# Kernel optimization log

Hardware: AMD Instinct MI355X
Metric: run time of the kernel (lower is better)

## Reference

```python
import jax, jax.numpy as jnp
import numpy as np

B, N, F, Tf, Tm, Df, Dm = 8, 128, 128, 64, 256, 32, 128
E, H, TE = 64, 128, 64  # node_emb_dim, hidden_dim, time_emb_dim


def setup_inputs() -> dict:
    key = jax.random.key(0)
    ks = jax.random.split(key, 16)
    s = 0.05
    return {
        'noisy_adj': jax.random.normal(ks[0], (B, N, N), jnp.float32),
        'node_feats': jax.random.normal(ks[1], (B, N, F), jnp.float32),
        'feat_fnirs': jax.random.normal(ks[2], (B, N, Tf, Df), jnp.float32),
        'feat_music': jax.random.normal(ks[3], (B, 1, Tm, Dm), jnp.float32),
        'g_pre': jax.random.normal(ks[4], (B, N, N), jnp.float32),
        'node_W': jax.random.normal(ks[5], (F, E), jnp.float32) * s,
        'node_b': jnp.zeros((E,), jnp.float32),
        'fnirs_W': jax.random.normal(ks[6], (Df, H), jnp.float32) * s,
        'fnirs_b': jnp.zeros((H,), jnp.float32),
        'music_W': jax.random.normal(ks[7], (Dm, H), jnp.float32) * s,
        'music_b': jnp.zeros((H,), jnp.float32),
        'mlp_W1': jax.random.normal(ks[8], (2 * E + 2 + H + TE, H), jnp.float32) * s,
        'mlp_b1': jnp.zeros((H,), jnp.float32),
        'mlp_W2': jax.random.normal(ks[9], (H, 1), jnp.float32) * s,
        'mlp_b2': jnp.zeros((1,), jnp.float32),
        't': jax.random.randint(ks[10], (B,), 0, Tf),
    }


def _time_embedding(t_idx):
    # sinusoidal timestep embedding -> [B, TE]
    half = TE // 2
    inv_freq = jnp.exp(-jnp.arange(half, dtype=jnp.float32) * (jnp.log(10000.0) / (half - 1)))
    freqs = t_idx.astype(jnp.float32)[:, None] * inv_freq  # [B, half]
    return jnp.concatenate([jnp.sin(freqs), jnp.cos(freqs)], axis=-1)


def _conditional(feat_fnirs, feat_music, fnirs_W, fnirs_b, music_W, music_b):
    # cross-attention: fNIRS timesteps attend over music timesteps
    q = feat_fnirs @ fnirs_W + fnirs_b          # [B,N,Tf,H]
    kv = feat_music @ music_W + music_b         # [B,1,Tm,H]
    scale = 1.0 / jnp.sqrt(jnp.float32(H))
    scores = jnp.einsum('bnfh,bomh->bnfm', q, kv) * scale  # [B,N,Tf,Tm]
    attn = jax.nn.softmax(scores, axis=-1)
    ctx = jnp.einsum('bnfm,bomh->bnfh', attn, kv)
    fused = q + ctx                              # [B,N,Tf,H]
    attn_weights = attn.mean(axis=1)             # mean across channels -> [B,Tf,Tm]
    ent = -(attn * jnp.log(attn + 1e-8)).sum(-1)
    attention_loss = ent.mean()
    return fused, attn_weights, attention_loss


def reference(noisy_adj, node_feats, feat_fnirs, feat_music, g_pre,
              node_W, node_b, fnirs_W, fnirs_b, music_W, music_b,
              mlp_W1, mlp_b1, mlp_W2, mlp_b2, t):
    h = node_feats @ node_W + node_b             # [B,N,E]

    fused, attn_weights, attention_loss = _conditional(
        feat_fnirs, feat_music, fnirs_W, fnirs_b, music_W, music_b)

    t_idx = jnp.clip(t, 0, fused.shape[2] - 1)
    # gather conditional state at diffusion step t -> [B,N,H]
    idx = jnp.broadcast_to(t_idx[:, None, None, None], (B, N, 1, H))
    cond_t = jnp.take_along_axis(fused, idx, axis=2)[:, :, 0, :]

    time_emb = _time_embedding(t_idx)            # [B,TE]

    # Fused edge MLP layer-1: split W1 along the concat axis instead of
    # materializing the [B,N,N,in_dim] concat tensor (same math).
    W1_hi = mlp_W1[:E]
    W1_hj = mlp_W1[E:2 * E]
    w_adj = mlp_W1[2 * E]          # [H]
    w_gpre = mlp_W1[2 * E + 1]     # [H]
    W1_cond = mlp_W1[2 * E + 2:2 * E + 2 + H]
    W1_time = mlp_W1[2 * E + 2 + H:]

    pre = ((h @ W1_hi)[:, :, None, :]            # h_i varies over row i
           + (h @ W1_hj)[:, None, :, :]          # h_j varies over col j
           + noisy_adj[..., None] * w_adj
           + g_pre[..., None] * w_gpre
           + (cond_t @ W1_cond)[:, None, :, :]   # cond broadcast over row i
           + (time_emb @ W1_time)[:, None, None, :]
           + mlp_b1)                             # [B,N,N,H]
    hid = jax.nn.relu(pre)
    noise_pred = (hid @ mlp_W2)[..., 0] + mlp_b2[0]  # [B,N,N]
    return noise_pred, attn_weights, attention_loss
```

## Files before the change

kernel.cpp:

```cpp
#include <hip/hip_runtime.h>
#include <hip/hip_bf16.h>

#define Bn  8
#define Nn  128
#define Fn  128
#define Tfn 64
#define Tmn 256
#define Dfn 32
#define Dmn 128
#define En  64
#define Hn  128
#define TEn 64

#define OUT_AW_OFF   (Bn*Nn*Nn)
#define OUT_LOSS_OFF (Bn*Nn*Nn + Bn*Tfn*Tmn)

#define WS_G     0
#define WS_BIAS  32768
#define WS_KVT   34816
#define WS_FWT   165888
#define WS_NWT   167936
#define WS_HIT   172032
#define WS_HJT   176128
#define WS_CONDT 180224
#define WS_TVEC  188416
#define WS_PI    189440
#define WS_PJ    320512
#define WS_LOSS  451584

#define SCALE 0.08838834764831845f

typedef __attribute__((ext_vector_type(8))) short short8;
typedef __attribute__((ext_vector_type(4))) float f32x4;

__device__ __forceinline__ unsigned short f2bf(float x) {
  __hip_bfloat16 h = __float2bfloat16(x);
  return __builtin_bit_cast(unsigned short, h);
}
__device__ __forceinline__ unsigned int pk2(float a, float b) {
  return (unsigned int)f2bf(a) | ((unsigned int)f2bf(b) << 16);
}

__global__ __launch_bounds__(128) void k_wprep(
    const float* __restrict__ W1, const float* __restrict__ b1,
    const float* __restrict__ node_W, const float* __restrict__ fnirs_W,
    const int* __restrict__ t,
    unsigned short* __restrict__ fwt, unsigned short* __restrict__ nwt,
    unsigned short* __restrict__ hit, unsigned short* __restrict__ hjt,
    unsigned short* __restrict__ condt, float* __restrict__ tvec,
    float* __restrict__ loss_acc)
{
  int blk = blockIdx.x, tid = threadIdx.x;
  if (blk < 8) {
    int b = blk;
    __shared__ float te_l[TEn];
    if (tid < TEn/2) {
      int tcl = min(max(t[b], 0), Tfn - 1);
      float fr = (float)tcl * __expf(-(float)tid * (logf(10000.f) / (TEn/2 - 1)));
      te_l[tid] = __sinf(fr);
      te_l[tid + TEn/2] = __cosf(fr);
    }
    __syncthreads();
    float a = b1[tid];
    #pragma unroll 8
    for (int u = 0; u < TEn; u++) a = fmaf(te_l[u], W1[(2*En + 2 + Hn + u)*Hn + tid], a);
    tvec[b*Hn + tid] = a;
    if (b == 0 && tid == 0) loss_acc[0] = 0.f;
  } else if (blk < 16) {
    int q = blk - 8;
    #pragma unroll 4
    for (int i = 0; i < 16; i++) {
      int k = q*16 + i;
      condt[k*Hn + tid] = f2bf(W1[(2*En + 2 + tid)*Hn + k]);
    }
  } else if (blk < 20) {
    int q = blk - 16;
    int e = tid & 63, kh = tid >> 6;
    #pragma unroll 4
    for (int i = 0; i < 16; i++) {
      int k = q*32 + kh*16 + i;
      hit[k*En + e] = f2bf(W1[e*Hn + k]);
    }
  } else if (blk < 24) {
    int q = blk - 20;
    int e = tid & 63, kh = tid >> 6;
    #pragma unroll 4
    for (int i = 0; i < 16; i++) {
      int k = q*32 + kh*16 + i;
      hjt[k*En + e] = f2bf(W1[(En + e)*Hn + k]);
    }
  } else if (blk < 32) {
    int q = blk - 24;
    int fl = tid & 15, eh = tid >> 4;
    #pragma unroll 4
    for (int i = 0; i < 8; i++) {
      int e = eh*8 + i;
      nwt[e*Fn + q*16 + fl] = f2bf(node_W[(q*16 + fl)*En + e]);
    }
  } else if (blk < 34) {
    int q = blk - 32;
    int d = tid & 31, hh = tid >> 5;
    #pragma unroll 4
    for (int i = 0; i < 16; i++) {
      int h = q*64 + hh*16 + i;
      fwt[h*Dfn + d] = f2bf(fnirs_W[d*Hn + h]);
    }
  }
}

__global__ __launch_bounds__(128) void k_kv(
    const float* __restrict__ feat_music, const float* __restrict__ music_W,
    const float* __restrict__ music_b, const float* __restrict__ fnirs_W,
    const float* __restrict__ fnirs_b, unsigned short* __restrict__ kvT,
    unsigned short* __restrict__ G_bf, float* __restrict__ bias)
{
  int b = blockIdx.x >> 8;
  int m = blockIdx.x & 255;
  int tid = threadIdx.x;
  __shared__ float fm_s[Dmn];
  __shared__ float kv_s[Hn];
  __shared__ float red[2];
  fm_s[tid] = feat_music[((size_t)b*Tmn + m)*Dmn + tid];
  __syncthreads();
  float a = music_b[tid];
  #pragma unroll 8
  for (int d = 0; d < Dmn; d++) a = fmaf(fm_s[d], music_W[d*Hn + tid], a);
  kv_s[tid] = a;
  kvT[((size_t)b*Hn + tid)*Tmn + m] = f2bf(a);
  float bp = fnirs_b[tid] * a;
  bp += __shfl_xor(bp, 32); bp += __shfl_xor(bp, 16); bp += __shfl_xor(bp, 8);
  bp += __shfl_xor(bp, 4);  bp += __shfl_xor(bp, 2);  bp += __shfl_xor(bp, 1);
  if ((tid & 63) == 0) red[tid >> 6] = bp;
  __syncthreads();
  int d = tid >> 2, qd = tid & 3;
  float g = 0.f;
  #pragma unroll 8
  for (int hh = 0; hh < 32; hh++) {
    int h = hh*4 + qd;
    g = fmaf(fnirs_W[d*Hn + h], kv_s[h], g);
  }
  g += __shfl_xor(g, 1); g += __shfl_xor(g, 2);
  if (qd == 0) G_bf[((size_t)b*Tmn + m)*Dfn + d] = f2bf(g * SCALE);
  if (tid == 0) bias[b*Tmn + m] = (red[0] + red[1]) * SCALE;
}

__global__ __launch_bounds__(256, 2) void k_attn(
    const float* __restrict__ feat_fnirs, const unsigned short* __restrict__ G_bf,
    const float* __restrict__ bias, float* __restrict__ aw_out,
    float* __restrict__ loss_acc)
{
  __shared__ unsigned short feat_l[Nn][40];
  __shared__ unsigned short G_l[Tmn][40];
  __shared__ float bias_l[Tmn];
  __shared__ float aw_l[4][Tmn];
  __shared__ float ent_l[4];

  int tid = threadIdx.x;
  int b = blockIdx.x >> 6, f = blockIdx.x & 63;

  {
    const uint4* gg = (const uint4*)(G_bf + (size_t)b*Tmn*Dfn);
    #pragma unroll
    for (int v0 = 0; v0 < 4; v0++) {
      int v = tid + v0*256;
      uint4 x = gg[v];
      int m = v >> 2, qt = v & 3;
      *((uint4*)&G_l[m][qt*8]) = x;
    }
    bias_l[tid] = bias[b*Tmn + tid];
    int n = tid >> 1, hf = tid & 1;
    const float* src = feat_fnirs + (((size_t)b*Nn + n)*Tfn + f)*Dfn + hf*16;
    float4 x0 = ((const float4*)src)[0];
    float4 x1 = ((const float4*)src)[1];
    float4 x2 = ((const float4*)src)[2];
    float4 x3 = ((const float4*)src)[3];
    uint4 pa, pb;
    pa.x = pk2(x0.x, x0.y); pa.y = pk2(x0.z, x0.w);
    pa.z = pk2(x1.x, x1.y); pa.w = pk2(x1.z, x1.w);
    pb.x = pk2(x2.x, x2.y); pb.y = pk2(x2.z, x2.w);
    pb.z = pk2(x3.x, x3.y); pb.w = pk2(x3.z, x3.w);
    uint4* dst = (uint4*)&feat_l[n][hf*16];
    dst[0] = pa; dst[1] = pb;
  }
  __syncthreads();

  int lane = tid & 63, wv = tid >> 6;
  int col = lane & 15, kq = lane >> 4;
  int n0 = wv * 32;

  short8 a0 = *(const short8*)&feat_l[n0 + col][kq*8];
  short8 a1 = *(const short8*)&feat_l[n0 + 16 + col][kq*8];

  float S0[4] = {0,0,0,0}, S1[4] = {0,0,0,0};
  float T0[4] = {0,0,0,0}, T1[4] = {0,0,0,0};
  float p0[16][4], p1[16][4];

  #pragma unroll
  for (int mt = 0; mt < 16; mt++) {
    short8 bfr = *(const short8*)&G_l[mt*16 + col][kq*8];
    float bv = bias_l[mt*16 + col];
    f32x4 c0 = __builtin_amdgcn_mfma_f32_16x16x32_bf16(a0, bfr, (f32x4){0.f,0.f,0.f,0.f}, 0, 0, 0);
    f32x4 c1 = __builtin_amdgcn_mfma_f32_16x16x32_bf16(a1, bfr, (f32x4){0.f,0.f,0.f,0.f}, 0, 0, 0);
    #pragma unroll
    for (int r = 0; r < 4; r++) {
      float sc = c0[r] + bv;
      float p = __expf(sc);
      S0[r] += p; T0[r] = fmaf(p, sc, T0[r]); p0[mt][r] = p;
      sc = c1[r] + bv;
      p = __expf(sc);
      S1[r] += p; T1[r] = fmaf(p, sc, T1[r]); p1[mt][r] = p;
    }
  }

  #pragma unroll
  for (int r = 0; r < 4; r++) {
    #pragma unroll
    for (int off = 1; off < 16; off <<= 1) {
      S0[r] += __shfl_xor(S0[r], off);
      S1[r] += __shfl_xor(S1[r], off);
      T0[r] += __shfl_xor(T0[r], off);
      T1[r] += __shfl_xor(T1[r], off);
    }
  }
  float i0v[4], i1v[4];
  #pragma unroll
  for (int r = 0; r < 4; r++) { i0v[r] = 1.f / S0[r]; i1v[r] = 1.f / S1[r]; }

  float ent = 0.f;
  if (col == 0) {
    #pragma unroll
    for (int r = 0; r < 4; r++) {
      ent += (__logf(S0[r]) - T0[r] * i0v[r]);
      ent += (__logf(S1[r]) - T1[r] * i1v[r]);
    }
  }
  ent += __shfl_xor(ent, 32); ent += __shfl_xor(ent, 16);
  ent += __shfl_xor(ent, 8);  ent += __shfl_xor(ent, 4);
  ent += __shfl_xor(ent, 2);  ent += __shfl_xor(ent, 1);
  if (lane == 0) ent_l[wv] = ent;

  #pragma unroll
  for (int mt = 0; mt < 16; mt++) {
    float a = 0.f;
    #pragma unroll
    for (int r = 0; r < 4; r++) {
      a = fmaf(p0[mt][r], i0v[r], a);
      a = fmaf(p1[mt][r], i1v[r], a);
    }
    a += __shfl_xor(a, 16);
    a += __shfl_xor(a, 32);
    if (lane < 16) aw_l[wv][mt*16 + lane] = a;
  }
  __syncthreads();

  float s = (aw_l[0][tid] + aw_l[1][tid]) + (aw_l[2][tid] + aw_l[3][tid]);
  aw_out[((size_t)b*Tfn + f)*Tmn + tid] = s * (1.f/(float)Nn);
  if (tid == 0)
    atomicAdd(loss_acc, (ent_l[0] + ent_l[1]) + (ent_l[2] + ent_l[3]));
}

__global__ __launch_bounds__(256) void k_cond(
    const float* __restrict__ feat_fnirs, const float* __restrict__ node_feats,
    const float* __restrict__ node_b, const int* __restrict__ t,
    const unsigned short* __restrict__ G_bf, const float* __restrict__ bias,
    const unsigned short* __restrict__ kvT, const unsigned short* __restrict__ fwt,
    const unsigned short* __restrict__ nwt, const unsigned short* __restrict__ hit,
    const unsigned short* __restrict__ hjt, const unsigned short* __restrict__ condt,
    const float* __restrict__ tvec, float* __restrict__ Pi, float* __restrict__ Pj)
{
  __shared__ unsigned short featT_l[16][40];
  __shared__ unsigned short A_l[16][264];
  __shared__ unsigned short nf_l[16][136];
  __shared__ unsigned short h_l[16][72];
  __shared__ unsigned short cond_l[16][136];
  __shared__ float sS[4][16];
  __shared__ float tvec_l[Hn];

  int tid = threadIdx.x;
  int b = blockIdx.x >> 3;
  int i0 = (blockIdx.x & 7) << 4;
  int tcl = min(max(t[b], 0), Tfn - 1);

  if (tid < 128) {
    int i = tid >> 3, c = (tid & 7) * 4;
    const float* src = feat_fnirs + (((size_t)b*Nn + i0 + i)*Tfn + tcl)*Dfn + c;
    float4 x = *(const float4*)src;
    *(unsigned int*)&featT_l[i][c]     = pk2(x.x, x.y);
    *(unsigned int*)&featT_l[i][c + 2] = pk2(x.z, x.w);
    tvec_l[tid] = tvec[b*Hn + tid];
  }
  {
    int i = tid >> 4, c = (tid & 15) * 8;
    const float* src = node_feats + ((size_t)b*Nn + i0 + i)*Fn + c;
    float4 x0 = ((const float4*)src)[0];
    float4 x1 = ((const float4*)src)[1];
    *(unsigned int*)&nf_l[i][c]     = pk2(x0.x, x0.y);
    *(unsigned int*)&nf_l[i][c + 2] = pk2(x0.z, x0.w);
    *(unsigned int*)&nf_l[i][c + 4] = pk2(x1.x, x1.y);
    *(unsigned int*)&nf_l[i][c + 6] = pk2(x1.z, x1.w);
  }
  __syncthreads();

  int lane = tid & 63, wv = tid >> 6;
  int col = lane & 15, kq = lane >> 4;

  short8 a_feat = *(const short8*)&featT_l[col][kq*8];

  float p[4][4];
  float Sp[4] = {0,0,0,0};
  #pragma unroll
  for (int mtl = 0; mtl < 4; mtl++) {
    int mt = wv*4 + mtl;
    short8 bg = *(const short8*)(G_bf + ((size_t)b*Tmn + mt*16 + col)*Dfn + kq*8);
    f32x4 c = __builtin_amdgcn_mfma_f32_16x16x32_bf16(a_feat, bg, (f32x4){0.f,0.f,0.f,0.f}, 0, 0, 0);
    float bv = bias[b*Tmn + mt*16 + col];
    #pragma unroll
    for (int r = 0; r < 4; r++) {
      float pp = __expf(c[r] + bv);
      p[mtl][r] = pp;
      Sp[r] += pp;
    }
  }
  #pragma unroll
  for (int r = 0; r < 4; r++) {
    float v = Sp[r];
    v += __shfl_xor(v, 1); v += __shfl_xor(v, 2);
    v += __shfl_xor(v, 4); v += __shfl_xor(v, 8);
    Sp[r] = v;
  }
  if (col == 0) {
    #pragma unroll
    for (int r = 0; r < 4; r++) sS[wv][kq*4 + r] = Sp[r];
  }
  __syncthreads();
  float invS[4];
  #pragma unroll
  for (int r = 0; r < 4; r++)
    invS[r] = 1.f / (sS[0][kq*4+r] + sS[1][kq*4+r] + sS[2][kq*4+r] + sS[3][kq*4+r]);
  #pragma unroll
  for (int mtl = 0; mtl < 4; mtl++) {
    #pragma unroll
    for (int r = 0; r < 4; r++)
      A_l[kq*4 + r][(wv*4 + mtl)*16 + col] = f2bf(p[mtl][r] * invS[r]);
  }
  __syncthreads();

  f32x4 accC0 = {0.f,0.f,0.f,0.f}, accC1 = {0.f,0.f,0.f,0.f};
  {
    int ct0 = wv*2, ct1 = wv*2 + 1;
    short8 bq0 = *(const short8*)(fwt + (size_t)(ct0*16 + col)*Dfn + kq*8);
    short8 bq1 = *(const short8*)(fwt + (size_t)(ct1*16 + col)*Dfn + kq*8);
    accC0 = __builtin_amdgcn_mfma_f32_16x16x32_bf16(a_feat, bq0, accC0, 0, 0, 0);
    accC1 = __builtin_amdgcn_mfma_f32_16x16x32_bf16(a_feat, bq1, accC1, 0, 0, 0);
    #pragma unroll
    for (int ks = 0; ks < 8; ks++) {
      short8 aA = *(const short8*)&A_l[col][ks*32 + kq*8];
      short8 bk0 = *(const short8*)(kvT + ((size_t)b*Hn + ct0*16 + col)*Tmn + ks*32 + kq*8);
      short8 bk1 = *(const short8*)(kvT + ((size_t)b*Hn + ct1*16 + col)*Tmn + ks*32 + kq*8);
      accC0 = __builtin_amdgcn_mfma_f32_16x16x32_bf16(aA, bk0, accC0, 0, 0, 0);
      accC1 = __builtin_amdgcn_mfma_f32_16x16x32_bf16(aA, bk1, accC1, 0, 0, 0);
    }
  }
  f32x4 accH = {0.f,0.f,0.f,0.f};
  #pragma unroll
  for (int ks = 0; ks < 4; ks++) {
    short8 aN = *(const short8*)&nf_l[col][ks*32 + kq*8];
    short8 bn = *(const short8*)(nwt + (size_t)(wv*16 + col)*Fn + ks*32 + kq*8);
    accH = __builtin_amdgcn_mfma_f32_16x16x32_bf16(aN, bn, accH, 0, 0, 0);
  }
  float nb = node_b[wv*16 + col];
  #pragma unroll
  for (int r = 0; r < 4; r++) {
    cond_l[kq*4 + r][(wv*2    )*16 + col] = f2bf(accC0[r]);
    cond_l[kq*4 + r][(wv*2 + 1)*16 + col] = f2bf(accC1[r]);
    h_l[kq*4 + r][wv*16 + col] = f2bf(accH[r] + nb);
  }
  __syncthreads();

  short8 aH[2];
  aH[0] = *(const short8*)&h_l[col][kq*8];
  aH[1] = *(const short8*)&h_l[col][32 + kq*8];
  #pragma unroll
  for (int ctl = 0; ctl < 2; ctl++) {
    int ct = wv*2 + ctl;
    f32x4 accPi = {0.f,0.f,0.f,0.f}, accPj = {0.f,0.f,0.f,0.f};
    #pragma unroll
    for (int ks = 0; ks < 2; ks++) {
      short8 bi_ = *(const short8*)(hit + (size_t)(ct*16 + col)*En + ks*32 + kq*8);
      short8 bj_ = *(const short8*)(hjt + (size_t)(ct*16 + col)*En + ks*32 + kq*8);
      accPi = __builtin_amdgcn_mfma_f32_16x16x32_bf16(aH[ks], bi_, accPi, 0, 0, 0);
      accPj = __builtin_amdgcn_mfma_f32_16x16x32_bf16(aH[ks], bj_, accPj, 0, 0, 0);
    }
    #pragma unroll
    for (int ks = 0; ks < 4; ks++) {
      short8 aC = *(const short8*)&cond_l[col][ks*32 + kq*8];
      short8 bc = *(const short8*)(condt + (size_t)(ct*16 + col)*Hn + ks*32 + kq*8);
      accPj = __builtin_amdgcn_mfma_f32_16x16x32_bf16(aC, bc, accPj, 0, 0, 0);
    }
    float tv = tvec_l[ct*16 + col];
    #pragma unroll
    for (int r = 0; r < 4; r++) {
      size_t row = (size_t)b*Nn + i0 + kq*4 + r;
      Pi[row*Hn + ct*16 + col] = accPi[r];
      Pj[row*Hn + ct*16 + col] = accPj[r] + tv;
    }
  }
}

__global__ __launch_bounds__(256) void k_edge(
    const float* __restrict__ adj, const float* __restrict__ gpre,
    const float* __restrict__ W1, const float* __restrict__ W2,
    const float* __restrict__ b2p, const float* __restrict__ Pi,
    const float* __restrict__ Pj, float* __restrict__ out,
    const float* __restrict__ loss_acc)
{
  int b  = blockIdx.x >> 6;
  int ib = (blockIdx.x >> 1) & 31;
  int jh = blockIdx.x & 1;
  int i0 = ib * 4;
  int tid = threadIdx.x;

  __shared__ float4 Pj_s4[64*32];
  __shared__ float4 Pi_s4[4*32];
  __shared__ float4 w2_s[32], wa_s[32], wg_s[32];

  {
    const float4* Pjg = (const float4*)(Pj + ((size_t)b*Nn + jh*64)*Hn);
    #pragma unroll
    for (int v0 = 0; v0 < 8; v0++) {
      int idx = tid + v0*256;
      int j = idx >> 5, c = idx & 31;
      Pj_s4[j*32 + (c ^ (j & 7))] = Pjg[j*32 + c];
    }
    if (tid < 128) {
      int r = tid >> 5, c = tid & 31;
      Pi_s4[r*32 + c] = ((const float4*)(Pi + ((size_t)b*Nn + i0 + r)*Hn))[c];
    } else if (tid < 160) {
      int c = tid - 128;
      w2_s[c] = ((const float4*)W2)[c];
      wa_s[c] = ((const float4*)(W1 + (2*En)*Hn))[c];
      wg_s[c] = ((const float4*)(W1 + (2*En + 1)*Hn))[c];
    }
  }
  __syncthreads();

  int r = tid >> 6, lane = tid & 63;
  int i = i0 + r, j = jh*64 + lane;
  float b2v = b2p[0];
  float adjv = adj [((size_t)b*Nn + i)*Nn + j];
  float gpv  = gpre[((size_t)b*Nn + i)*Nn + j];
  float a0 = 0.f, a1 = 0.f, a2 = 0.f, a3 = 0.f;
  #pragma unroll
  for (int c = 0; c < 32; c++) {
    float4 pj = Pj_s4[lane*32 + (c ^ (lane & 7))];
    float4 pi = Pi_s4[r*32 + c];
    float4 wa = wa_s[c], wg = wg_s[c], w2 = w2_s[c];
    float e0 = pi.x + pj.x + adjv*wa.x + gpv*wg.x;
    float e1 = pi.y + pj.y + adjv*wa.y + gpv*wg.y;
    float e2 = pi.z + pj.z + adjv*wa.z + gpv*wg.z;
    float e3 = pi.w + pj.w + adjv*wa.w + gpv*wg.w;
    a0 = fmaf(fmaxf(e0, 0.f), w2.x, a0);
    a1 = fmaf(fmaxf(e1, 0.f), w2.y, a1);
    a2 = fmaf(fmaxf(e2, 0.f), w2.z, a2);
    a3 = fmaf(fmaxf(e3, 0.f), w2.w, a3);
  }
  out[((size_t)b*Nn + i)*Nn + j] = (a0 + a1) + (a2 + a3) + b2v;

  if (blockIdx.x == 0 && tid == 0)
    out[OUT_LOSS_OFF] = loss_acc[0] * (1.f / (float)(Bn*Nn*Tfn));
}

extern "C" void kernel_launch(void* const* d_in, const int* in_sizes, int n_in,
                              void* d_out, int out_size, void* d_ws, size_t ws_size,
                              hipStream_t stream) {
  (void)in_sizes; (void)n_in; (void)out_size; (void)ws_size;
  const float* noisy_adj  = (const float*)d_in[0];
  const float* node_feats = (const float*)d_in[1];
  const float* feat_fnirs = (const float*)d_in[2];
  const float* feat_music = (const float*)d_in[3];
  const float* g_pre      = (const float*)d_in[4];
  const float* node_W     = (const float*)d_in[5];
  const float* node_b     = (const float*)d_in[6];
  const float* fnirs_W    = (const float*)d_in[7];
  const float* fnirs_b    = (const float*)d_in[8];
  const float* music_W    = (const float*)d_in[9];
  const float* music_b    = (const float*)d_in[10];
  const float* mlp_W1     = (const float*)d_in[11];
  const float* mlp_b1     = (const float*)d_in[12];
  const float* mlp_W2     = (const float*)d_in[13];
  const float* mlp_b2     = (const float*)d_in[14];
  const int*   t          = (const int*)d_in[15];

  float* out = (float*)d_out;
  float* ws = (float*)d_ws;
  unsigned short* g_ws    = (unsigned short*)(ws + WS_G);
  float*          bias_ws = ws + WS_BIAS;
  unsigned short* kvt_ws  = (unsigned short*)(ws + WS_KVT);
  unsigned short* fwt_ws  = (unsigned short*)(ws + WS_FWT);
  unsigned short* nwt_ws  = (unsigned short*)(ws + WS_NWT);
  unsigned short* hit_ws  = (unsigned short*)(ws + WS_HIT);
  unsigned short* hjt_ws  = (unsigned short*)(ws + WS_HJT);
  unsigned short* cndt_ws = (unsigned short*)(ws + WS_CONDT);
  float*          tvec_ws = ws + WS_TVEC;
  float*          Pi_ws   = ws + WS_PI;
  float*          Pj_ws   = ws + WS_PJ;
  float*          loss_ws = ws + WS_LOSS;

  k_wprep<<<34,         128, 0, stream>>>(mlp_W1, mlp_b1, node_W, fnirs_W, t,
                                          fwt_ws, nwt_ws, hit_ws, hjt_ws, cndt_ws,
                                          tvec_ws, loss_ws);
  k_kv   <<<Bn*Tmn,     128, 0, stream>>>(feat_music, music_W, music_b, fnirs_W,
                                          fnirs_b, kvt_ws, g_ws, bias_ws);
  k_attn <<<Bn*Tfn,     256, 0, stream>>>(feat_fnirs, g_ws, bias_ws,
                                          out + OUT_AW_OFF, loss_ws);
  k_cond <<<Bn*(Nn/16), 256, 0, stream>>>(feat_fnirs, node_feats, node_b, t,
                                          g_ws, bias_ws, kvt_ws, fwt_ws, nwt_ws,
                                          hit_ws, hjt_ws, cndt_ws, tvec_ws,
                                          Pi_ws, Pj_ws);
  k_edge <<<512,        256, 0, stream>>>(noisy_adj, g_pre, mlp_W1, mlp_W2, mlp_b2,
                                          Pi_ws, Pj_ws, out, loss_ws);
}
```

Measured before the change: 137.1 us.

## Merge independent kernels into combined launches and widen edge LDS swizzle

The five launches become three. The weight-prep blocks and the music KV projection blocks now share one grid, and the attention-weights blocks share a grid with the conditional-state blocks, with shared memory overlaid through a union. The aim is to cut launch overhead and let independent work run concurrently on the GPU. The edge kernel's Pj shared-memory XOR swizzle now uses all 5 lane bits instead of 3 to reduce LDS bank conflicts. Merging attention with conditional state puts both branches under one register and occupancy budget, and the union forces the larger shared-memory footprint on every block.

```diff
diff --git a/kernel.cpp b/kernel.cpp
--- a/kernel.cpp
+++ b/kernel.cpp
@@ -41,19 +41,56 @@
   return (unsigned int)f2bf(a) | ((unsigned int)f2bf(b) << 16);
 }
 
-__global__ __launch_bounds__(128) void k_wprep(
+__global__ __launch_bounds__(128) void k_prep(
+    const float* __restrict__ feat_music, const float* __restrict__ music_W,
+    const float* __restrict__ music_b, const float* __restrict__ fnirs_W,
+    const float* __restrict__ fnirs_b,
     const float* __restrict__ W1, const float* __restrict__ b1,
-    const float* __restrict__ node_W, const float* __restrict__ fnirs_W,
-    const int* __restrict__ t,
+    const float* __restrict__ node_W, const int* __restrict__ t,
+    unsigned short* __restrict__ kvT, unsigned short* __restrict__ G_bf,
+    float* __restrict__ bias,
     unsigned short* __restrict__ fwt, unsigned short* __restrict__ nwt,
     unsigned short* __restrict__ hit, unsigned short* __restrict__ hjt,
     unsigned short* __restrict__ condt, float* __restrict__ tvec,
     float* __restrict__ loss_acc)
 {
-  int blk = blockIdx.x, tid = threadIdx.x;
+  __shared__ float fm_s[Dmn];
+  __shared__ float kv_s[Hn];
+  __shared__ float red[2];
+  __shared__ float te_l[TEn];
+  int tid = threadIdx.x;
+
+  if (blockIdx.x < 2048) {
+    int b = blockIdx.x >> 8;
+    int m = blockIdx.x & 255;
+    fm_s[tid] = feat_music[((size_t)b*Tmn + m)*Dmn + tid];
+    __syncthreads();
+    float a = music_b[tid];
+    #pragma unroll 8
+    for (int d = 0; d < Dmn; d++) a = fmaf(fm_s[d], music_W[d*Hn + tid], a);
+    kv_s[tid] = a;
+    kvT[((size_t)b*Hn + tid)*Tmn + m] = f2bf(a);
+    float bp = fnirs_b[tid] * a;
+    bp += __shfl_xor(bp, 32); bp += __shfl_xor(bp, 16); bp += __shfl_xor(bp, 8);
+    bp += __shfl_xor(bp, 4);  bp += __shfl_xor(bp, 2);  bp += __shfl_xor(bp, 1);
+    if ((tid & 63) == 0) red[tid >> 6] = bp;
+    __syncthreads();
+    int d = tid >> 2, qd = tid & 3;
+    float g = 0.f;
+    #pragma unroll 8
+    for (int hh = 0; hh < 32; hh++) {
+      int h = hh*4 + qd;
+      g = fmaf(fnirs_W[d*Hn + h], kv_s[h], g);
+    }
+    g += __shfl_xor(g, 1); g += __shfl_xor(g, 2);
+    if (qd == 0) G_bf[((size_t)b*Tmn + m)*Dfn + d] = f2bf(g * SCALE);
+    if (tid == 0) bias[b*Tmn + m] = (red[0] + red[1]) * SCALE;
+    return;
+  }
+
+  int blk = blockIdx.x - 2048;
   if (blk < 8) {
     int b = blk;
-    __shared__ float te_l[TEn];
     if (tid < TEn/2) {
       int tcl = min(max(t[b], 0), Tfn - 1);
       float fr = (float)tcl * __expf(-(float)tid * (logf(10000.f) / (TEn/2 - 1)));
@@ -108,203 +145,171 @@
   }
 }
 
-__global__ __launch_bounds__(128) void k_kv(
-    const float* __restrict__ feat_music, const float* __restrict__ music_W,
-    const float* __restrict__ music_b, const float* __restrict__ fnirs_W,
-    const float* __restrict__ fnirs_b, unsigned short* __restrict__ kvT,
-    unsigned short* __restrict__ G_bf, float* __restrict__ bias)
-{
-  int b = blockIdx.x >> 8;
-  int m = blockIdx.x & 255;
-  int tid = threadIdx.x;
-  __shared__ float fm_s[Dmn];
-  __shared__ float kv_s[Hn];
-  __shared__ float red[2];
-  fm_s[tid] = feat_music[((size_t)b*Tmn + m)*Dmn + tid];
-  __syncthreads();
-  float a = music_b[tid];
-  #pragma unroll 8
-  for (int d = 0; d < Dmn; d++) a = fmaf(fm_s[d], music_W[d*Hn + tid], a);
-  kv_s[tid] = a;
-  kvT[((size_t)b*Hn + tid)*Tmn + m] = f2bf(a);
-  float bp = fnirs_b[tid] * a;
-  bp += __shfl_xor(bp, 32); bp += __shfl_xor(bp, 16); bp += __shfl_xor(bp, 8);
-  bp += __shfl_xor(bp, 4);  bp += __shfl_xor(bp, 2);  bp += __shfl_xor(bp, 1);
-  if ((tid & 63) == 0) red[tid >> 6] = bp;
-  __syncthreads();
-  int d = tid >> 2, qd = tid & 3;
-  float g = 0.f;
-  #pragma unroll 8
-  for (int hh = 0; hh < 32; hh++) {
-    int h = hh*4 + qd;
-    g = fmaf(fnirs_W[d*Hn + h], kv_s[h], g);
-  }
-  g += __shfl_xor(g, 1); g += __shfl_xor(g, 2);
-  if (qd == 0) G_bf[((size_t)b*Tmn + m)*Dfn + d] = f2bf(g * SCALE);
-  if (tid == 0) bias[b*Tmn + m] = (red[0] + red[1]) * SCALE;
-}
-
-__global__ __launch_bounds__(256, 2) void k_attn(
-    const float* __restrict__ feat_fnirs, const unsigned short* __restrict__ G_bf,
-    const float* __restrict__ bias, float* __restrict__ aw_out,
-    float* __restrict__ loss_acc)
-{
-  __shared__ unsigned short feat_l[Nn][40];
-  __shared__ unsigned short G_l[Tmn][40];
-  __shared__ float bias_l[Tmn];
-  __shared__ float aw_l[4][Tmn];
-  __shared__ float ent_l[4];
-
-  int tid = threadIdx.x;
-  int b = blockIdx.x >> 6, f = blockIdx.x & 63;
-
-  {
-    const uint4* gg = (const uint4*)(G_bf + (size_t)b*Tmn*Dfn);
-    #pragma unroll
-    for (int v0 = 0; v0 < 4; v0++) {
-      int v = tid + v0*256;
-      uint4 x = gg[v];
-      int m = v >> 2, qt = v & 3;
-      *((uint4*)&G_l[m][qt*8]) = x;
-    }
-    bias_l[tid] = bias[b*Tmn + tid];
-    int n = tid >> 1, hf = tid & 1;
-    const float* src = feat_fnirs + (((size_t)b*Nn + n)*Tfn + f)*Dfn + hf*16;
-    float4 x0 = ((const float4*)src)[0];
-    float4 x1 = ((const float4*)src)[1];
-    float4 x2 = ((const float4*)src)[2];
-    float4 x3 = ((const float4*)src)[3];
-    uint4 pa, pb;
-    pa.x = pk2(x0.x, x0.y); pa.y = pk2(x0.z, x0.w);
-    pa.z = pk2(x1.x, x1.y); pa.w = pk2(x1.z, x1.w);
-    pb.x = pk2(x2.x, x2.y); pb.y = pk2(x2.z, x2.w);
-    pb.z = pk2(x3.x, x3.y); pb.w = pk2(x3.z, x3.w);
-    uint4* dst = (uint4*)&feat_l[n][hf*16];
-    dst[0] = pa; dst[1] = pb;
-  }
-  __syncthreads();
-
-  int lane = tid & 63, wv = tid >> 6;
-  int col = lane & 15, kq = lane >> 4;
-  int n0 = wv * 32;
-
-  short8 a0 = *(const short8*)&feat_l[n0 + col][kq*8];
-  short8 a1 = *(const short8*)&feat_l[n0 + 16 + col][kq*8];
-
-  float S0[4] = {0,0,0,0}, S1[4] = {0,0,0,0};
-  float T0[4] = {0,0,0,0}, T1[4] = {0,0,0,0};
-  float p0[16][4], p1[16][4];
-
-  #pragma unroll
-  for (int mt = 0; mt < 16; mt++) {
-    short8 bfr = *(const short8*)&G_l[mt*16 + col][kq*8];
-    float bv = bias_l[mt*16 + col];
-    f32x4 c0 = __builtin_amdgcn_mfma_f32_16x16x32_bf16(a0, bfr, (f32x4){0.f,0.f,0.f,0.f}, 0, 0, 0);
-    f32x4 c1 = __builtin_amdgcn_mfma_f32_16x16x32_bf16(a1, bfr, (f32x4){0.f,0.f,0.f,0.f}, 0, 0, 0);
-    #pragma unroll
-    for (int r = 0; r < 4; r++) {
-      float sc = c0[r] + bv;
-      float p = __expf(sc);
-      S0[r] += p; T0[r] = fmaf(p, sc, T0[r]); p0[mt][r] = p;
-      sc = c1[r] + bv;
-      p = __expf(sc);
-      S1[r] += p; T1[r] = fmaf(p, sc, T1[r]); p1[mt][r] = p;
-    }
-  }
-
-  #pragma unroll
-  for (int r = 0; r < 4; r++) {
-    #pragma unroll
-    for (int off = 1; off < 16; off <<= 1) {
-      S0[r] += __shfl_xor(S0[r], off);
-      S1[r] += __shfl_xor(S1[r], off);
-      T0[r] += __shfl_xor(T0[r], off);
-      T1[r] += __shfl_xor(T1[r], off);
-    }
-  }
-  float i0v[4], i1v[4];
-  #pragma unroll
-  for (int r = 0; r < 4; r++) { i0v[r] = 1.f / S0[r]; i1v[r] = 1.f / S1[r]; }
-
-  float ent = 0.f;
-  if (col == 0) {
-    #pragma unroll
-    for (int r = 0; r < 4; r++) {
-      ent += (__logf(S0[r]) - T0[r] * i0v[r]);
-      ent += (__logf(S1[r]) - T1[r] * i1v[r]);
-    }
-  }
-  ent += __shfl_xor(ent, 32); ent += __shfl_xor(ent, 16);
-  ent += __shfl_xor(ent, 8);  ent += __shfl_xor(ent, 4);
-  ent += __shfl_xor(ent, 2);  ent += __shfl_xor(ent, 1);
-  if (lane == 0) ent_l[wv] = ent;
-
-  #pragma unroll
-  for (int mt = 0; mt < 16; mt++) {
-    float a = 0.f;
-    #pragma unroll
-    for (int r = 0; r < 4; r++) {
-      a = fmaf(p0[mt][r], i0v[r], a);
-      a = fmaf(p1[mt][r], i1v[r], a);
-    }
-    a += __shfl_xor(a, 16);
-    a += __shfl_xor(a, 32);
-    if (lane < 16) aw_l[wv][mt*16 + lane] = a;
-  }
-  __syncthreads();
-
-  float s = (aw_l[0][tid] + aw_l[1][tid]) + (aw_l[2][tid] + aw_l[3][tid]);
-  aw_out[((size_t)b*Tfn + f)*Tmn + tid] = s * (1.f/(float)Nn);
-  if (tid == 0)
-    atomicAdd(loss_acc, (ent_l[0] + ent_l[1]) + (ent_l[2] + ent_l[3]));
-}
-
-__global__ __launch_bounds__(256) void k_cond(
+struct SmemAttn {
+  unsigned short feat_l[Nn][40];
+  unsigned short G_l[Tmn][40];
+  float bias_l[Tmn];
+  float aw_l[4][Tmn];
+  float ent_l[4];
+};
+struct SmemCond {
+  unsigned short featT_l[16][40];
+  unsigned short A_l[16][264];
+  unsigned short nf_l[16][136];
+  unsigned short h_l[16][72];
+  unsigned short cond_l[16][136];
+  float sS[4][16];
+  float tvec_l[Hn];
+};
+union __align__(16) SmemK2 {
+  SmemAttn a;
+  SmemCond c;
+};
+
+__global__ __launch_bounds__(256, 2) void k_attn_cond(
     const float* __restrict__ feat_fnirs, const float* __restrict__ node_feats,
     const float* __restrict__ node_b, const int* __restrict__ t,
     const unsigned short* __restrict__ G_bf, const float* __restrict__ bias,
     const unsigned short* __restrict__ kvT, const unsigned short* __restrict__ fwt,
     const unsigned short* __restrict__ nwt, const unsigned short* __restrict__ hit,
     const unsigned short* __restrict__ hjt, const unsigned short* __restrict__ condt,
-    const float* __restrict__ tvec, float* __restrict__ Pi, float* __restrict__ Pj)
+    const float* __restrict__ tvec, float* __restrict__ Pi, float* __restrict__ Pj,
+    float* __restrict__ aw_out, float* __restrict__ loss_acc)
 {
-  __shared__ unsigned short featT_l[16][40];
-  __shared__ unsigned short A_l[16][264];
-  __shared__ unsigned short nf_l[16][136];
-  __shared__ unsigned short h_l[16][72];
-  __shared__ unsigned short cond_l[16][136];
-  __shared__ float sS[4][16];
-  __shared__ float tvec_l[Hn];
-
+  __shared__ SmemK2 smem;
   int tid = threadIdx.x;
-  int b = blockIdx.x >> 3;
-  int i0 = (blockIdx.x & 7) << 4;
+  int lane = tid & 63, wv = tid >> 6;
+  int col = lane & 15, kq = lane >> 4;
+
+  if (blockIdx.x < 512) {
+    int b = blockIdx.x >> 6, f = blockIdx.x & 63;
+    {
+      const uint4* gg = (const uint4*)(G_bf + (size_t)b*Tmn*Dfn);
+      #pragma unroll
+      for (int v0 = 0; v0 < 4; v0++) {
+        int v = tid + v0*256;
+        uint4 x = gg[v];
+        int m = v >> 2, qt = v & 3;
+        *((uint4*)&smem.a.G_l[m][qt*8]) = x;
+      }
+      smem.a.bias_l[tid] = bias[b*Tmn + tid];
+      int n = tid >> 1, hf = tid & 1;
+      const float* src = feat_fnirs + (((size_t)b*Nn + n)*Tfn + f)*Dfn + hf*16;
+      float4 x0 = ((const float4*)src)[0];
+      float4 x1 = ((const float4*)src)[1];
+      float4 x2 = ((const float4*)src)[2];
+      float4 x3 = ((const float4*)src)[3];
+      uint4 pa, pb;
+      pa.x = pk2(x0.x, x0.y); pa.y = pk2(x0.z, x0.w);
+      pa.z = pk2(x1.x, x1.y); pa.w = pk2(x1.z, x1.w);
+      pb.x = pk2(x2.x, x2.y); pb.y = pk2(x2.z, x2.w);
+      pb.z = pk2(x3.x, x3.y); pb.w = pk2(x3.z, x3.w);
+      uint4* dst = (uint4*)&smem.a.feat_l[n][hf*16];
+      dst[0] = pa; dst[1] = pb;
+    }
+    __syncthreads();
+
+    int n0 = wv * 32;
+    short8 a0 = *(const short8*)&smem.a.feat_l[n0 + col][kq*8];
+    short8 a1 = *(const short8*)&smem.a.feat_l[n0 + 16 + col][kq*8];
+
+    float S0[4] = {0,0,0,0}, S1[4] = {0,0,0,0};
+    float T0[4] = {0,0,0,0}, T1[4] = {0,0,0,0};
+    float p0[16][4], p1[16][4];
+
+    #pragma unroll
+    for (int mt = 0; mt < 16; mt++) {
+      short8 bfr = *(const short8*)&smem.a.G_l[mt*16 + col][kq*8];
+      float bv = smem.a.bias_l[mt*16 + col];
+      f32x4 c0 = __builtin_amdgcn_mfma_f32_16x16x32_bf16(a0, bfr, (f32x4){0.f,0.f,0.f,0.f}, 0, 0, 0);
+      f32x4 c1 = __builtin_amdgcn_mfma_f32_16x16x32_bf16(a1, bfr, (f32x4){0.f,0.f,0.f,0.f}, 0, 0, 0);
+      #pragma unroll
+      for (int r = 0; r < 4; r++) {
+        float sc = c0[r] + bv;
+        float p = __expf(sc);
+        S0[r] += p; T0[r] = fmaf(p, sc, T0[r]); p0[mt][r] = p;
+        sc = c1[r] + bv;
+        p = __expf(sc);
+        S1[r] += p; T1[r] = fmaf(p, sc, T1[r]); p1[mt][r] = p;
+      }
+    }
+
+    #pragma unroll
+    for (int r = 0; r < 4; r++) {
+      #pragma unroll
+      for (int off = 1; off < 16; off <<= 1) {
+        S0[r] += __shfl_xor(S0[r], off);
+        S1[r] += __shfl_xor(S1[r], off);
+        T0[r] += __shfl_xor(T0[r], off);
+        T1[r] += __shfl_xor(T1[r], off);
+      }
+    }
+    float i0v[4], i1v[4];
+    #pragma unroll
+    for (int r = 0; r < 4; r++) { i0v[r] = 1.f / S0[r]; i1v[r] = 1.f / S1[r]; }
+
+    float ent = 0.f;
+    if (col == 0) {
+      #pragma unroll
+      for (int r = 0; r < 4; r++) {
+        ent += (__logf(S0[r]) - T0[r] * i0v[r]);
+        ent += (__logf(S1[r]) - T1[r] * i1v[r]);
+      }
+    }
+    ent += __shfl_xor(ent, 32); ent += __shfl_xor(ent, 16);
+    ent += __shfl_xor(ent, 8);  ent += __shfl_xor(ent, 4);
+    ent += __shfl_xor(ent, 2);  ent += __shfl_xor(ent, 1);
+    if (lane == 0) smem.a.ent_l[wv] = ent;
+
+    #pragma unroll
+    for (int mt = 0; mt < 16; mt++) {
+      float a = 0.f;
+      #pragma unroll
+      for (int r = 0; r < 4; r++) {
+        a = fmaf(p0[mt][r], i0v[r], a);
+        a = fmaf(p1[mt][r], i1v[r], a);
+      }
+      a += __shfl_xor(a, 16);
+      a += __shfl_xor(a, 32);
+      if (lane < 16) smem.a.aw_l[wv][mt*16 + lane] = a;
+    }
+    __syncthreads();
+
+    float s = (smem.a.aw_l[0][tid] + smem.a.aw_l[1][tid]) +
+              (smem.a.aw_l[2][tid] + smem.a.aw_l[3][tid]);
+    aw_out[((size_t)b*Tfn + f)*Tmn + tid] = s * (1.f/(float)Nn);
+    if (tid == 0)
+      atomicAdd(loss_acc, (smem.a.ent_l[0] + smem.a.ent_l[1]) +
+                          (smem.a.ent_l[2] + smem.a.ent_l[3]));
+    return;
+  }
+
+  int blk = blockIdx.x - 512;
+  int b = blk >> 3;
+  int i0 = (blk & 7) << 4;
   int tcl = min(max(t[b], 0), Tfn - 1);
 
   if (tid < 128) {
     int i = tid >> 3, c = (tid & 7) * 4;
     const float* src = feat_fnirs + (((size_t)b*Nn + i0 + i)*Tfn + tcl)*Dfn + c;
     float4 x = *(const float4*)src;
-    *(unsigned int*)&featT_l[i][c]     = pk2(x.x, x.y);
-    *(unsigned int*)&featT_l[i][c + 2] = pk2(x.z, x.w);
-    tvec_l[tid] = tvec[b*Hn + tid];
+    *(unsigned int*)&smem.c.featT_l[i][c]     = pk2(x.x, x.y);
+    *(unsigned int*)&smem.c.featT_l[i][c + 2] = pk2(x.z, x.w);
+    smem.c.tvec_l[tid] = tvec[b*Hn + tid];
   }
   {
     int i = tid >> 4, c = (tid & 15) * 8;
     const float* src = node_feats + ((size_t)b*Nn + i0 + i)*Fn + c;
     float4 x0 = ((const float4*)src)[0];
     float4 x1 = ((const float4*)src)[1];
-    *(unsigned int*)&nf_l[i][c]     = pk2(x0.x, x0.y);
-    *(unsigned int*)&nf_l[i][c + 2] = pk2(x0.z, x0.w);
-    *(unsigned int*)&nf_l[i][c + 4] = pk2(x1.x, x1.y);
-    *(unsigned int*)&nf_l[i][c + 6] = pk2(x1.z, x1.w);
+    *(unsigned int*)&smem.c.nf_l[i][c]     = pk2(x0.x, x0.y);
+    *(unsigned int*)&smem.c.nf_l[i][c + 2] = pk2(x0.z, x0.w);
+    *(unsigned int*)&smem.c.nf_l[i][c + 4] = pk2(x1.x, x1.y);
+    *(unsigned int*)&smem.c.nf_l[i][c + 6] = pk2(x1.z, x1.w);
   }
   __syncthreads();
 
-  int lane = tid & 63, wv = tid >> 6;
-  int col = lane & 15, kq = lane >> 4;
-
-  short8 a_feat = *(const short8*)&featT_l[col][kq*8];
+  short8 a_feat = *(const short8*)&smem.c.featT_l[col][kq*8];
 
   float p[4][4];
   float Sp[4] = {0,0,0,0};
@@ -330,18 +335,19 @@
   }
   if (col == 0) {
     #pragma unroll
-    for (int r = 0; r < 4; r++) sS[wv][kq*4 + r] = Sp[r];
+    for (int r = 0; r < 4; r++) smem.c.sS[wv][kq*4 + r] = Sp[r];
   }
   __syncthreads();
   float invS[4];
   #pragma unroll
   for (int r = 0; r < 4; r++)
-    invS[r] = 1.f / (sS[0][kq*4+r] + sS[1][kq*4+r] + sS[2][kq*4+r] + sS[3][kq*4+r]);
+    invS[r] = 1.f / (smem.c.sS[0][kq*4+r] + smem.c.sS[1][kq*4+r] +
+                     smem.c.sS[2][kq*4+r] + smem.c.sS[3][kq*4+r]);
   #pragma unroll
   for (int mtl = 0; mtl < 4; mtl++) {
     #pragma unroll
     for (int r = 0; r < 4; r++)
-      A_l[kq*4 + r][(wv*4 + mtl)*16 + col] = f2bf(p[mtl][r] * invS[r]);
+      smem.c.A_l[kq*4 + r][(wv*4 + mtl)*16 + col] = f2bf(p[mtl][r] * invS[r]);
   }
   __syncthreads();
 
@@ -354,7 +360,7 @@
     accC1 = __builtin_amdgcn_mfma_f32_16x16x32_bf16(a_feat, bq1, accC1, 0, 0, 0);
     #pragma unroll
     for (int ks = 0; ks < 8; ks++) {
-      short8 aA = *(const short8*)&A_l[col][ks*32 + kq*8];
+      short8 aA = *(const short8*)&smem.c.A_l[col][ks*32 + kq*8];
       short8 bk0 = *(const short8*)(kvT + ((size_t)b*Hn + ct0*16 + col)*Tmn + ks*32 + kq*8);
       short8 bk1 = *(const short8*)(kvT + ((size_t)b*Hn + ct1*16 + col)*Tmn + ks*32 + kq*8);
       accC0 = __builtin_amdgcn_mfma_f32_16x16x32_bf16(aA, bk0, accC0, 0, 0, 0);
@@ -364,22 +370,22 @@
   f32x4 accH = {0.f,0.f,0.f,0.f};
   #pragma unroll
   for (int ks = 0; ks < 4; ks++) {
-    short8 aN = *(const short8*)&nf_l[col][ks*32 + kq*8];
+    short8 aN = *(const short8*)&smem.c.nf_l[col][ks*32 + kq*8];
     short8 bn = *(const short8*)(nwt + (size_t)(wv*16 + col)*Fn + ks*32 + kq*8);
     accH = __builtin_amdgcn_mfma_f32_16x16x32_bf16(aN, bn, accH, 0, 0, 0);
   }
   float nb = node_b[wv*16 + col];
   #pragma unroll
   for (int r = 0; r < 4; r++) {
-    cond_l[kq*4 + r][(wv*2    )*16 + col] = f2bf(accC0[r]);
-    cond_l[kq*4 + r][(wv*2 + 1)*16 + col] = f2bf(accC1[r]);
-    h_l[kq*4 + r][wv*16 + col] = f2bf(accH[r] + nb);
+    smem.c.cond_l[kq*4 + r][(wv*2    )*16 + col] = f2bf(accC0[r]);
+    smem.c.cond_l[kq*4 + r][(wv*2 + 1)*16 + col] = f2bf(accC1[r]);
+    smem.c.h_l[kq*4 + r][wv*16 + col] = f2bf(accH[r] + nb);
   }
   __syncthreads();
 
   short8 aH[2];
-  aH[0] = *(const short8*)&h_l[col][kq*8];
-  aH[1] = *(const short8*)&h_l[col][32 + kq*8];
+  aH[0] = *(const short8*)&smem.c.h_l[col][kq*8];
+  aH[1] = *(const short8*)&smem.c.h_l[col][32 + kq*8];
   #pragma unroll
   for (int ctl = 0; ctl < 2; ctl++) {
     int ct = wv*2 + ctl;
@@ -393,11 +399,11 @@
     }
     #pragma unroll
     for (int ks = 0; ks < 4; ks++) {
-      short8 aC = *(const short8*)&cond_l[col][ks*32 + kq*8];
+      short8 aC = *(const short8*)&smem.c.cond_l[col][ks*32 + kq*8];
       short8 bc = *(const short8*)(condt + (size_t)(ct*16 + col)*Hn + ks*32 + kq*8);
       accPj = __builtin_amdgcn_mfma_f32_16x16x32_bf16(aC, bc, accPj, 0, 0, 0);
     }
-    float tv = tvec_l[ct*16 + col];
+    float tv = smem.c.tvec_l[ct*16 + col];
     #pragma unroll
     for (int r = 0; r < 4; r++) {
       size_t row = (size_t)b*Nn + i0 + kq*4 + r;
@@ -430,7 +436,7 @@
     for (int v0 = 0; v0 < 8; v0++) {
       int idx = tid + v0*256;
       int j = idx >> 5, c = idx & 31;
-      Pj_s4[j*32 + (c ^ (j & 7))] = Pjg[j*32 + c];
+      Pj_s4[j*32 + (c ^ (j & 31))] = Pjg[j*32 + c];
     }
     if (tid < 128) {
       int r = tid >> 5, c = tid & 31;
@@ -452,7 +458,7 @@
   float a0 = 0.f, a1 = 0.f, a2 = 0.f, a3 = 0.f;
   #pragma unroll
   for (int c = 0; c < 32; c++) {
-    float4 pj = Pj_s4[lane*32 + (c ^ (lane & 7))];
+    float4 pj = Pj_s4[lane*32 + (c ^ (lane & 31))];
     float4 pi = Pi_s4[r*32 + c];
     float4 wa = wa_s[c], wg = wg_s[c], w2 = w2_s[c];
     float e0 = pi.x + pj.x + adjv*wa.x + gpv*wg.x;
@@ -506,17 +512,14 @@
   float*          Pj_ws   = ws + WS_PJ;
   float*          loss_ws = ws + WS_LOSS;
 
-  k_wprep<<<34,         128, 0, stream>>>(mlp_W1, mlp_b1, node_W, fnirs_W, t,
-                                          fwt_ws, nwt_ws, hit_ws, hjt_ws, cndt_ws,
-                                          tvec_ws, loss_ws);
-  k_kv   <<<Bn*Tmn,     128, 0, stream>>>(feat_music, music_W, music_b, fnirs_W,
-                                          fnirs_b, kvt_ws, g_ws, bias_ws);
-  k_attn <<<Bn*Tfn,     256, 0, stream>>>(feat_fnirs, g_ws, bias_ws,
-                                          out + OUT_AW_OFF, loss_ws);
-  k_cond <<<Bn*(Nn/16), 256, 0, stream>>>(feat_fnirs, node_feats, node_b, t,
-                                          g_ws, bias_ws, kvt_ws, fwt_ws, nwt_ws,
-                                          hit_ws, hjt_ws, cndt_ws, tvec_ws,
-                                          Pi_ws, Pj_ws);
-  k_edge <<<512,        256, 0, stream>>>(noisy_adj, g_pre, mlp_W1, mlp_W2, mlp_b2,
-                                          Pi_ws, Pj_ws, out, loss_ws);
+  k_prep     <<<2082, 128, 0, stream>>>(feat_music, music_W, music_b, fnirs_W,
+                                        fnirs_b, mlp_W1, mlp_b1, node_W, t,
+                                        kvt_ws, g_ws, bias_ws, fwt_ws, nwt_ws,
+                                        hit_ws, hjt_ws, cndt_ws, tvec_ws, loss_ws);
+  k_attn_cond<<<576,  256, 0, stream>>>(feat_fnirs, node_feats, node_b, t,
+                                        g_ws, bias_ws, kvt_ws, fwt_ws, nwt_ws,
+                                        hit_ws, hjt_ws, cndt_ws, tvec_ws,
+                                        Pi_ws, Pj_ws, out + OUT_AW_OFF, loss_ws);
+  k_edge     <<<512,  256, 0, stream>>>(noisy_adj, g_pre, mlp_W1, mlp_W2, mlp_b2,
+                                        Pi_ws, Pj_ws, out, loss_ws);
 }
```

Result: faster. 131.4 us (-4.1%).
